# Kernel tuning notes

Measured on AMD Instinct MI355X. Metric: run time of the kernel, lower is better.

The kernel has to match this reference:

```python
import jax, jax.numpy as jnp
import numpy as np

WINDOW = 34
WIN = WINDOW * 3 - 2  # 100, sliding window size


def _windowed_sum(a, w):
    # a: [B, T] -> sliding-window sums of length w: [B, T - w + 1]
    c = jnp.cumsum(a, axis=-1)
    c = jnp.pad(c, ((0, 0), (1, 0)))  # prepend zero so c[..., i] = sum(a[..., :i])
    return c[..., w:] - c[..., :-w]


def setup_inputs() -> dict:
    key = jax.random.key(0)
    x = jax.random.normal(key, (512, 2, 32768), dtype=jnp.float32)
    return {"x": x}


def reference(x):
    w = jnp.float32(WIN)
    x1 = x[:, 0, :]  # [B, T]
    x2 = x[:, 1, :]
    s1 = _windowed_sum(x1, WIN)
    s2 = _windowed_sum(x2, WIN)
    s11 = _windowed_sum(x1 * x1, WIN)
    s22 = _windowed_sum(x2 * x2, WIN)
    s12 = _windowed_sum(x1 * x2, WIN)
    # Pearson: sum((x1-m1)*(x2-m2)) / (sqrt(sum (x1-m1)^2) * sqrt(sum (x2-m2)^2))
    cov = s12 - s1 * s2 / w
    v1 = s11 - s1 * s1 / w
    v2 = s22 - s2 * s2 / w
    corr = cov / (jnp.sqrt(v1) * jnp.sqrt(v2))  # [B, N]
    # attention_generation: subtract batch mean, keep positive part
    avg = corr.mean(axis=0)                     # [N]
    r = corr - avg
    attentions = r * (r > 0).astype(r.dtype)
    return attentions  # original returns (attentions, None)
```

## Files before the change

kernel.cpp:

```cpp
#include <hip/hip_runtime.h>

#define LROW 32768
#define NROW 512
#define WIN 100
#define NC (LROW - WIN + 1)
#define NT1 256
#define T 8
#define CT (T * NT1)
#define NTILE ((NC + CT - 1) / CT)
#define G 4
#define RG (NROW / G)
#define SEG (CT + WIN - 1)
#define SEGP (SEG + (SEG >> 3) + 2)

__device__ __forceinline__ int pad8(int e) { return e + (e >> 3); }

__global__ __launch_bounds__(NT1, 4)
void swc_pass1(const float* __restrict__ x, float* __restrict__ colsum,
               float* __restrict__ out)
{
    __shared__ float lds1[SEGP];
    __shared__ float lds2[SEGP];

    const int tile = (int)blockIdx.x % NTILE;
    const int rg   = (int)blockIdx.x / NTILE;
    const int j0   = tile * CT;
    const int seglen = min(SEG, LROW - j0);
    const int ncols  = min(CT, NC - j0);
    const int tid  = (int)threadIdx.x;
    const int c0   = tid * T;
    const int pbase = 9 * tid;
    const bool active = c0 < ncols;

    float acc[T];
    #pragma unroll
    for (int m = 0; m < T; ++m) acc[m] = 0.0f;

    const int r0 = rg * G;
    for (int r = r0; r < r0 + G; ++r) {
        const float* __restrict__ p1 = x + ((size_t)(2 * r) + 0) * LROW + j0;
        const float* __restrict__ p2 = x + ((size_t)(2 * r) + 1) * LROW + j0;
        __syncthreads();
        const int nvec = seglen >> 2;
        for (int i = tid; i < nvec; i += NT1) {
            float4 v1 = ((const float4*)p1)[i];
            float4 v2 = ((const float4*)p2)[i];
            int b = 4 * i + (i >> 1);
            lds1[b + 0] = v1.x; lds1[b + 1] = v1.y; lds1[b + 2] = v1.z; lds1[b + 3] = v1.w;
            lds2[b + 0] = v2.x; lds2[b + 1] = v2.y; lds2[b + 2] = v2.z; lds2[b + 3] = v2.w;
        }
        for (int e = (nvec << 2) + tid; e < seglen; e += NT1) {
            lds1[pad8(e)] = p1[e];
            lds2[pad8(e)] = p2[e];
        }
        __syncthreads();

        float rout[T];
        if (active) {
            float s1 = 0.f, s2 = 0.f, s11 = 0.f, s22 = 0.f, s12 = 0.f;
            #pragma unroll
            for (int k = 0; k < WIN; ++k) {
                float a = lds1[pbase + k + (k >> 3)];
                float b = lds2[pbase + k + (k >> 3)];
                s1 += a; s2 += b;
                s11 = fmaf(a, a, s11);
                s22 = fmaf(b, b, s22);
                s12 = fmaf(a, b, s12);
            }
            #pragma unroll
            for (int m = 0; m < T; ++m) {
                if (m > 0) {
                    const int eo = m - 1, ei = m - 1 + WIN;
                    float a_o = lds1[pbase + eo];
                    float b_o = lds2[pbase + eo];
                    float a_i = lds1[pbase + ei + (ei >> 3)];
                    float b_i = lds2[pbase + ei + (ei >> 3)];
                    s1 += a_i - a_o;
                    s2 += b_i - b_o;
                    s11 += fmaf(a_i, a_i, -(a_o * a_o));
                    s22 += fmaf(b_i, b_i, -(b_o * b_o));
                    s12 += fmaf(a_i, b_i, -(a_o * b_o));
                }
                const float invw = 1.0f / (float)WIN;
                float cov = fmaf(-(s1 * invw), s2, s12);
                float v1v = fmaf(-(s1 * invw), s1, s11);
                float v2v = fmaf(-(s2 * invw), s2, s22);
                float corr = cov * rsqrtf(v1v * v2v);
                rout[m] = corr;
                if (c0 + m < ncols) acc[m] += corr;
            }
        } else {
            #pragma unroll
            for (int m = 0; m < T; ++m) rout[m] = 0.0f;
        }

        __syncthreads();
        #pragma unroll
        for (int m = 0; m < T; ++m) lds1[pbase + m] = rout[m];
        __syncthreads();
        float* __restrict__ orow = out + (size_t)r * NC + j0;
        for (int e = tid; e < ncols; e += NT1) {
            orow[e] = lds1[pad8(e)];
        }
    }

    if (active) {
        #pragma unroll
        for (int m = 0; m < T; ++m) {
            if (c0 + m < ncols) atomicAdd(&colsum[j0 + c0 + m], acc[m]);
        }
    }
}

__global__ __launch_bounds__(256)
void swc_pass2(float* __restrict__ out, const float* __restrict__ colsum)
{
    const int row = (int)blockIdx.y;
    const int j0  = (int)blockIdx.x * 4096;
    float* __restrict__ orow = out + (size_t)row * NC;
    #pragma unroll
    for (int k = 0; k < 16; ++k) {
        int col = j0 + k * 256 + (int)threadIdx.x;
        if (col < NC) {
            float avg = colsum[col] * (1.0f / (float)NROW);
            float v = orow[col] - avg;
            orow[col] = fmaxf(v, 0.0f);
        }
    }
}

extern "C" void kernel_launch(void* const* d_in, const int* in_sizes, int n_in,
                              void* d_out, int out_size, void* d_ws, size_t ws_size,
                              hipStream_t stream) {
    const float* x = (const float*)d_in[0];
    float* out = (float*)d_out;
    float* colsum = (float*)d_ws;

    hipMemsetAsync(colsum, 0, NC * sizeof(float), stream);
    swc_pass1<<<dim3(NTILE * RG), dim3(NT1), 0, stream>>>(x, colsum, out);
    swc_pass2<<<dim3(8, NROW), dim3(256), 0, stream>>>(out, colsum);
}
```

Before: 311.7 us.

## Move column-sum out of pass1 into separate reduce kernel, widen per-thread tile

Pass1 now processes 16 columns per thread with a new LDS padding scheme and writes each correlation directly to global memory. It no longer stages results through LDS or accumulates per-column atomics. A new reduce kernel re-reads the full output to build column sums with row-split atomics, and pass2 is flattened to float4 accesses. This removes two barriers and the LDS staging per row and reduces atomic contention, but adds a full extra read of the output and leaves pass1's global stores uncoalesced, since each thread writes a strided run of 16 floats.

Measured after the change: 296.1 us. 1.05x faster.

```diff
diff --git a/kernel.cpp b/kernel.cpp
--- a/kernel.cpp
+++ b/kernel.cpp
@@ -5,19 +5,22 @@
 #define WIN 100
 #define NC (LROW - WIN + 1)
 #define NT1 256
-#define T 8
+#define T 16
 #define CT (T * NT1)
 #define NTILE ((NC + CT - 1) / CT)
 #define G 4
 #define RG (NROW / G)
 #define SEG (CT + WIN - 1)
-#define SEGP (SEG + (SEG >> 3) + 2)
+#define SEGP (SEG + 3 * (SEG >> 4) + 4)
+#define N_TOT (NROW * NC)
+#define N4 (N_TOT / 4)
+#define RSPLIT 32
+#define RCHUNK (NROW / RSPLIT)
 
-__device__ __forceinline__ int pad8(int e) { return e + (e >> 3); }
+__device__ __forceinline__ int pad3(int e) { return e + 3 * (e >> 4); }
 
 __global__ __launch_bounds__(NT1, 4)
-void swc_pass1(const float* __restrict__ x, float* __restrict__ colsum,
-               float* __restrict__ out)
+void swc_pass1(const float* __restrict__ x, float* __restrict__ out)
 {
     __shared__ float lds1[SEGP];
     __shared__ float lds2[SEGP];
@@ -29,15 +32,11 @@
     const int ncols  = min(CT, NC - j0);
     const int tid  = (int)threadIdx.x;
     const int c0   = tid * T;
-    const int pbase = 9 * tid;
-    const bool active = c0 < ncols;
-
-    float acc[T];
-    #pragma unroll
-    for (int m = 0; m < T; ++m) acc[m] = 0.0f;
+    const int pbase = 19 * tid;
 
     const int r0 = rg * G;
-    for (int r = r0; r < r0 + G; ++r) {
+    for (int rr = 0; rr < G; ++rr) {
+        const int r = r0 + rr;
         const float* __restrict__ p1 = x + ((size_t)(2 * r) + 0) * LROW + j0;
         const float* __restrict__ p2 = x + ((size_t)(2 * r) + 1) * LROW + j0;
         __syncthreads();
@@ -45,86 +44,87 @@
         for (int i = tid; i < nvec; i += NT1) {
             float4 v1 = ((const float4*)p1)[i];
             float4 v2 = ((const float4*)p2)[i];
-            int b = 4 * i + (i >> 1);
+            int b = 4 * i + 3 * (i >> 2);
             lds1[b + 0] = v1.x; lds1[b + 1] = v1.y; lds1[b + 2] = v1.z; lds1[b + 3] = v1.w;
             lds2[b + 0] = v2.x; lds2[b + 1] = v2.y; lds2[b + 2] = v2.z; lds2[b + 3] = v2.w;
         }
         for (int e = (nvec << 2) + tid; e < seglen; e += NT1) {
-            lds1[pad8(e)] = p1[e];
-            lds2[pad8(e)] = p2[e];
+            lds1[pad3(e)] = p1[e];
+            lds2[pad3(e)] = p2[e];
         }
         __syncthreads();
 
-        float rout[T];
-        if (active) {
-            float s1 = 0.f, s2 = 0.f, s11 = 0.f, s22 = 0.f, s12 = 0.f;
-            #pragma unroll
-            for (int k = 0; k < WIN; ++k) {
-                float a = lds1[pbase + k + (k >> 3)];
-                float b = lds2[pbase + k + (k >> 3)];
-                s1 += a; s2 += b;
-                s11 = fmaf(a, a, s11);
-                s22 = fmaf(b, b, s22);
-                s12 = fmaf(a, b, s12);
-            }
-            #pragma unroll
-            for (int m = 0; m < T; ++m) {
-                if (m > 0) {
-                    const int eo = m - 1, ei = m - 1 + WIN;
-                    float a_o = lds1[pbase + eo];
-                    float b_o = lds2[pbase + eo];
-                    float a_i = lds1[pbase + ei + (ei >> 3)];
-                    float b_i = lds2[pbase + ei + (ei >> 3)];
-                    s1 += a_i - a_o;
-                    s2 += b_i - b_o;
-                    s11 += fmaf(a_i, a_i, -(a_o * a_o));
-                    s22 += fmaf(b_i, b_i, -(b_o * b_o));
-                    s12 += fmaf(a_i, b_i, -(a_o * b_o));
-                }
-                const float invw = 1.0f / (float)WIN;
-                float cov = fmaf(-(s1 * invw), s2, s12);
-                float v1v = fmaf(-(s1 * invw), s1, s11);
-                float v2v = fmaf(-(s2 * invw), s2, s22);
-                float corr = cov * rsqrtf(v1v * v2v);
-                rout[m] = corr;
-                if (c0 + m < ncols) acc[m] += corr;
-            }
-        } else {
-            #pragma unroll
-            for (int m = 0; m < T; ++m) rout[m] = 0.0f;
+        float s1 = 0.f, s2 = 0.f, s11 = 0.f, s22 = 0.f, s12 = 0.f;
+        #pragma unroll
+        for (int k = 0; k < WIN; ++k) {
+            float a = lds1[pbase + k + 3 * (k >> 4)];
+            float b = lds2[pbase + k + 3 * (k >> 4)];
+            s1 += a; s2 += b;
+            s11 = fmaf(a, a, s11);
+            s22 = fmaf(b, b, s22);
+            s12 = fmaf(a, b, s12);
         }
-
-        __syncthreads();
-        #pragma unroll
-        for (int m = 0; m < T; ++m) lds1[pbase + m] = rout[m];
-        __syncthreads();
         float* __restrict__ orow = out + (size_t)r * NC + j0;
-        for (int e = tid; e < ncols; e += NT1) {
-            orow[e] = lds1[pad8(e)];
-        }
-    }
-
-    if (active) {
         #pragma unroll
         for (int m = 0; m < T; ++m) {
-            if (c0 + m < ncols) atomicAdd(&colsum[j0 + c0 + m], acc[m]);
+            if (m > 0) {
+                const int ko = m - 1;
+                const int kn = m - 1 + WIN;
+                float a_o = lds1[pbase + ko];
+                float b_o = lds2[pbase + ko];
+                float a_i = lds1[pbase + kn + 3 * (kn >> 4)];
+                float b_i = lds2[pbase + kn + 3 * (kn >> 4)];
+                s1 += a_i - a_o;
+                s2 += b_i - b_o;
+                s11 += fmaf(a_i, a_i, -(a_o * a_o));
+                s22 += fmaf(b_i, b_i, -(b_o * b_o));
+                s12 += fmaf(a_i, b_i, -(a_o * b_o));
+            }
+            const float invw = 1.0f / (float)WIN;
+            float cov = fmaf(-(s1 * invw), s2, s12);
+            float v1v = fmaf(-(s1 * invw), s1, s11);
+            float v2v = fmaf(-(s2 * invw), s2, s22);
+            float corr = cov * rsqrtf(v1v * v2v);
+            if (c0 + m < ncols) orow[c0 + m] = corr;
         }
     }
 }
 
 __global__ __launch_bounds__(256)
+void swc_reduce(const float* __restrict__ out, float* __restrict__ colsum)
+{
+    int col = (int)blockIdx.x * 256 + (int)threadIdx.x;
+    if (col >= NC) return;
+    const int r0 = (int)blockIdx.y * RCHUNK;
+    float s = 0.f;
+    #pragma unroll
+    for (int i = 0; i < RCHUNK; ++i)
+        s += out[(size_t)(r0 + i) * NC + col];
+    atomicAdd(&colsum[col], s);
+}
+
+__global__ __launch_bounds__(256)
 void swc_pass2(float* __restrict__ out, const float* __restrict__ colsum)
 {
-    const int row = (int)blockIdx.y;
-    const int j0  = (int)blockIdx.x * 4096;
-    float* __restrict__ orow = out + (size_t)row * NC;
+    const float inv = 1.0f / (float)NROW;
+    int base = (int)blockIdx.x * 2048 + (int)threadIdx.x;
     #pragma unroll
-    for (int k = 0; k < 16; ++k) {
-        int col = j0 + k * 256 + (int)threadIdx.x;
-        if (col < NC) {
-            float avg = colsum[col] * (1.0f / (float)NROW);
-            float v = orow[col] - avg;
-            orow[col] = fmaxf(v, 0.0f);
+    for (int v = 0; v < 8; ++v) {
+        int i4 = base + v * 256;
+        if (i4 < N4) {
+            float4 o = ((float4*)out)[i4];
+            int idx = i4 << 2;
+            int row = (int)((unsigned)idx / (unsigned)NC);
+            int col = idx - row * NC;
+            int c1 = col + 1, c2 = col + 2, c3 = col + 3;
+            if (c1 >= NC) c1 -= NC;
+            if (c2 >= NC) c2 -= NC;
+            if (c3 >= NC) c3 -= NC;
+            o.x = fmaxf(o.x - colsum[col] * inv, 0.f);
+            o.y = fmaxf(o.y - colsum[c1] * inv, 0.f);
+            o.z = fmaxf(o.z - colsum[c2] * inv, 0.f);
+            o.w = fmaxf(o.w - colsum[c3] * inv, 0.f);
+            ((float4*)out)[i4] = o;
         }
     }
 }
@@ -137,6 +137,7 @@
     float* colsum = (float*)d_ws;
 
     hipMemsetAsync(colsum, 0, NC * sizeof(float), stream);
-    swc_pass1<<<dim3(NTILE * RG), dim3(NT1), 0, stream>>>(x, colsum, out);
-    swc_pass2<<<dim3(8, NROW), dim3(256), 0, stream>>>(out, colsum);
+    swc_pass1<<<dim3(NTILE * RG), dim3(NT1), 0, stream>>>(x, out);
+    swc_reduce<<<dim3((NC + 255) / 256, RSPLIT), dim3(256), 0, stream>>>(out, colsum);
+    swc_pass2<<<dim3((N4 + 2047) / 2048), dim3(256), 0, stream>>>(out, colsum);
 }
```
